# Kernel optimization log

Measured on AMD Instinct MI355X. Metric: run time of the kernel, lower is better.

## Reference

```python
import jax, jax.numpy as jnp
import numpy as np

D_MODEL = 1024
DFF = 4096
SPARSITY = 0.5
EPS = 1e-6


def layer_norm(x, gamma, beta):
    mu = jnp.mean(x, axis=-1, keepdims=True)
    var = jnp.mean(jnp.square(x - mu), axis=-1, keepdims=True)
    return (x - mu) * jax.lax.rsqrt(var + EPS) * gamma + beta


def setup_inputs() -> dict:
    key = jax.random.key(0)
    ks = jax.random.split(key, 8)
    B, S, d, f = 4, 2048, D_MODEL, DFF
    s = 1.0 / np.sqrt(d)
    return {
        "x": jax.random.normal(ks[0], (B, S, d), dtype=jnp.float32),
        "Wq": jax.random.normal(ks[1], (d, d), dtype=jnp.float32) * s,
        "bq": jnp.zeros((d,), jnp.float32),
        "Wk": jax.random.normal(ks[2], (d, d), dtype=jnp.float32) * s,
        "bk": jnp.zeros((d,), jnp.float32),
        "Wv": jax.random.normal(ks[3], (d, d), dtype=jnp.float32) * s,
        "bv": jnp.zeros((d,), jnp.float32),
        "W1": jax.random.normal(ks[4], (d, f), dtype=jnp.float32) * s,
        "b1": jnp.zeros((f,), jnp.float32),
        "W2": jax.random.normal(ks[5], (f, d), dtype=jnp.float32) * (1.0 / np.sqrt(f)),
        "b2": jnp.zeros((d,), jnp.float32),
        "gamma1": jnp.ones((d,), jnp.float32),
        "beta1": jnp.zeros((d,), jnp.float32),
        "gamma2": jnp.ones((d,), jnp.float32),
        "beta2": jnp.zeros((d,), jnp.float32),
    }


def reference(x, Wq, bq, Wk, bk, Wv, bv, W1, b1, W2, b2, gamma1, beta1, gamma2, beta2):
    B, S, d = x.shape
    q = x @ Wq + bq
    k = x @ Wk + bk
    v = x @ Wv + bv
    # scores: [B, S, S], scaled by sqrt(d_model)
    scores = jnp.einsum("bqd,bkd->bqk", q, k) / jnp.sqrt(jnp.float32(d))
    # top-k sparsification: keep scores >= row-wise k-th largest, else 0
    topk = int(SPARSITY * S)
    top_vals = jax.lax.top_k(scores, topk)[0]  # sorted descending
    threshold = top_vals[..., -1:]
    sparse_scores = jnp.where(scores >= threshold, scores, jnp.zeros_like(scores))
    attn = jax.nn.softmax(sparse_scores, axis=-1)
    attn_out = jnp.einsum("bqk,bkd->bqd", attn, v)
    out1 = layer_norm(x + attn_out, gamma1, beta1)
    ffn = jax.nn.relu(out1 @ W1 + b1) @ W2 + b2
    return layer_norm(out1 + ffn, gamma2, beta2)
```

## Files before the change

kernel.cpp:

```cpp
#include <hip/hip_runtime.h>
#include <cstdint>

typedef unsigned short u16;
typedef __attribute__((ext_vector_type(8))) short s16x8;
typedef __attribute__((ext_vector_type(4))) unsigned short u16x4;
typedef __attribute__((ext_vector_type(4))) float f32x4;

__device__ __forceinline__ u16 f2bf(float f) {
  union { float f; uint32_t u; } c; c.f = f;
  uint32_t r = c.u + 0x7FFFu + ((c.u >> 16) & 1u);
  return (u16)(r >> 16);
}
__device__ __forceinline__ float bf2f(u16 b) {
  union { uint32_t u; float f; } c; c.u = ((uint32_t)b) << 16;
  return c.f;
}
__device__ __forceinline__ float wave_sum_f(float v) {
#pragma unroll
  for (int o = 32; o > 0; o >>= 1) v += __shfl_xor(v, o);
  return v;
}
__device__ __forceinline__ float wave_max_f(float v) {
#pragma unroll
  for (int o = 32; o > 0; o >>= 1) v = fmaxf(v, __shfl_xor(v, o));
  return v;
}
__device__ __forceinline__ void gload16(const u16* g, u16* l) {
  __builtin_amdgcn_global_load_lds(
      (const __attribute__((address_space(1))) unsigned int*)g,
      (__attribute__((address_space(3))) unsigned int*)l,
      16, 0, 0);
}

__global__ __launch_bounds__(256)
void cast_f32_bf16(const float* __restrict__ in, u16* __restrict__ out) {
  long i = ((long)blockIdx.x * 256 + threadIdx.x) * 4;
  f32x4 v = *(const f32x4*)(in + i);
  u16x4 o;
#pragma unroll
  for (int j = 0; j < 4; ++j) o[j] = f2bf(v[j]);
  *(u16x4*)(out + i) = o;
}

__global__ __launch_bounds__(256)
void concat3(const float* __restrict__ a, const float* __restrict__ b,
             const float* __restrict__ c, float* __restrict__ o) {
  int i = blockIdx.x * 256 + threadIdx.x;
  o[i] = i < 1024 ? a[i] : (i < 2048 ? b[i - 1024] : c[i - 2048]);
}

__global__ __launch_bounds__(256)
void transpose_cast_f32_bf16(const float* __restrict__ in, u16* __restrict__ out,
                             int R, int C) {
  __shared__ float tile[32][33];
  int r0 = blockIdx.y * 32, c0 = blockIdx.x * 32;
  int tid = threadIdx.x;
  int tr = tid >> 3, tc4 = (tid & 7) * 4;
  f32x4 v = *(const f32x4*)(in + (long)(r0 + tr) * C + c0 + tc4);
#pragma unroll
  for (int j = 0; j < 4; ++j) tile[tr][tc4 + j] = v[j];
  __syncthreads();
  u16x4 o;
#pragma unroll
  for (int j = 0; j < 4; ++j) o[j] = f2bf(tile[tc4 + j][tr]);
  *(u16x4*)(out + (long)(c0 + tr) * R + r0 + tc4) = o;
}

__global__ __launch_bounds__(256)
void transpose_bf16(const u16* __restrict__ in, u16* __restrict__ out,
                    int R, int C, int in_rs, long in_batch, long out_batch) {
  __shared__ u16 tile[32][36];
  const long zin = (long)blockIdx.z * in_batch;
  const long zout = (long)blockIdx.z * out_batch;
  int r0 = blockIdx.y * 32, c0 = blockIdx.x * 32;
  int tid = threadIdx.x;
  int tr = tid >> 3, tc4 = (tid & 7) * 4;
  u16x4 v = *(const u16x4*)(in + zin + (long)(r0 + tr) * in_rs + c0 + tc4);
#pragma unroll
  for (int j = 0; j < 4; ++j) tile[tr][tc4 + j] = v[j];
  __syncthreads();
  u16x4 o;
#pragma unroll
  for (int j = 0; j < 4; ++j) o[j] = tile[tc4 + j][tr];
  *(u16x4*)(out + zout + (long)(c0 + tr) * R + r0 + tc4) = o;
}

#define TBM 256
#define TBK 64

enum { EPI_BF16_BIAS = 0, EPI_BF16_SCALE = 1, EPI_F32 = 2,
       EPI_RELU_BF16_BIAS = 3, EPI_F32_BIAS_RESID = 4 };

#define QUAD(MFA)                                                             \
  _Pragma("unroll")                                                           \
  for (int mf = (MFA); mf < (MFA) + 2; ++mf)                                  \
    _Pragma("unroll")                                                         \
    for (int nf = 0; nf < 4; ++nf) {                                          \
      acc[mf][nf] = __builtin_amdgcn_mfma_f32_16x16x32_bf16(                  \
          af[mf][0], bfr[nf][0], acc[mf][nf], 0, 0, 0);                       \
      acc[mf][nf] = __builtin_amdgcn_mfma_f32_16x16x32_bf16(                  \
          af[mf][1], bfr[nf][1], acc[mf][nf], 0, 0, 0);                       \
    }

template <int BN_, int EPI>
__global__ __launch_bounds__(512, 2)
void gemm2p(const u16* __restrict__ A, const u16* __restrict__ Bt,
            const float* __restrict__ bias, const float* __restrict__ resid,
            void* __restrict__ Cout, int M, int N, int K, int lda, int ldb,
            int tx, int ty, long long batchA, long long batchB, long long batchC,
            float scale) {
  constexpr int MF = (BN_ == 256) ? 8 : 4;
  constexpr int NBI = BN_ / 128;
  __shared__ u16 As[2][TBM * TBK];
  __shared__ u16 Bs[2][BN_ * TBK];

  const int nwg = gridDim.x;
  const int orig = blockIdx.x;
  const int q = nwg >> 3, r = nwg & 7;
  const int xcd = orig & 7, idx = orig >> 3;
  const int wg = (xcd < r ? xcd * (q + 1) : r * (q + 1) + (xcd - r) * q) + idx;
  const int bx = wg % tx;
  const int tmp = wg / tx;
  const int by = tmp % ty;
  const int b  = tmp / ty;

  const u16* Ab = A + (long)b * batchA;
  const u16* Bb = Bt + (long)b * batchB;
  const int row0 = by * TBM;
  const int col0 = bx * BN_;
  const int tid = threadIdx.x;
  const int lane = tid & 63, wid = tid >> 6;
  const int wm = (BN_ == 256) ? (wid >> 2) : (wid >> 1);
  const int wn = (BN_ == 256) ? (wid & 3) : (wid & 1);
  const int rowW = (BN_ == 256) ? wm * 128 : wm * 64;
  const int l15 = lane & 15, g = lane >> 4;

  const int sr = lane >> 3;
  const int sc = ((lane & 7) ^ sr) * 8;
  const int wrow = wid * 8 + sr;

  const int c0 = ((0 + g) ^ (l15 & 7)) * 8;
  const int c1 = ((4 + g) ^ (l15 & 7)) * 8;

  auto stageA = [&](int h, int kt, int bf_) {
#pragma unroll
    for (int j = 0; j < 2; ++j)
      gload16(Ab + (size_t)(row0 + h * 128 + j * 64 + wrow) * lda + kt * TBK + sc,
              &As[bf_][(h * 128 + j * 64 + wid * 8) * TBK]);
  };
  auto stageB = [&](int h, int kt, int bf_) {
#pragma unroll
    for (int j = 0; j < NBI; ++j)
      gload16(Bb + (size_t)(col0 + h * (BN_ / 2) + j * 64 + wrow) * ldb + kt * TBK + sc,
              &Bs[bf_][(h * (BN_ / 2) + j * 64 + wid * 8) * TBK]);
  };

  s16x8 af[MF][2];
  s16x8 bfr[4][2];
  f32x4 acc[MF][4] = {};
  const int nt = K / TBK;

  stageA(0, 0, 0); stageA(1, 0, 0);
  stageB(0, 0, 0); stageB(1, 0, 0);
  if (nt > 1) {
    stageA(0, 1, 1); stageA(1, 1, 1);
    stageB(0, 1, 1); stageB(1, 1, 1);
    if constexpr (BN_ == 256) asm volatile("s_waitcnt vmcnt(8)" ::: "memory");
    else                      asm volatile("s_waitcnt vmcnt(6)" ::: "memory");
  } else {
    asm volatile("s_waitcnt vmcnt(0)" ::: "memory");
  }
  __builtin_amdgcn_s_barrier();

  for (int t = 0; t < nt; ++t) {
    const int cur = t & 1;
    const u16* Asc = &As[cur][0];
    const u16* Bsc = &Bs[cur][0];

#pragma unroll
    for (int nf = 0; nf < 4; ++nf) {
      const int rb = (wn * 64 + nf * 16 + l15) * TBK;
      bfr[nf][0] = *(const s16x8*)(Bsc + rb + c0);
      bfr[nf][1] = *(const s16x8*)(Bsc + rb + c1);
    }
#pragma unroll
    for (int mf = 0; mf < MF; ++mf) {
      const int rb = (rowW + mf * 16 + l15) * TBK;
      af[mf][0] = *(const s16x8*)(Asc + rb + c0);
      af[mf][1] = *(const s16x8*)(Asc + rb + c1);
    }
    asm volatile("s_waitcnt lgkmcnt(0)" ::: "memory");
    __builtin_amdgcn_sched_barrier(0);
    __builtin_amdgcn_s_barrier();

    if (t + 2 < nt) { stageB(0, t + 2, cur); stageB(1, t + 2, cur); }
    __builtin_amdgcn_s_setprio(1);
    QUAD(0)
    if constexpr (MF == 8) { QUAD(2) }
    __builtin_amdgcn_s_setprio(0);
    if (t + 2 < nt) { stageA(0, t + 2, cur); stageA(1, t + 2, cur); }
    __builtin_amdgcn_s_setprio(1);
    if constexpr (MF == 8) { QUAD(4) QUAD(6) }
    else                   { QUAD(2) }
    __builtin_amdgcn_s_setprio(0);

    if (t + 1 < nt) {
      if (t + 2 < nt) {
        if constexpr (BN_ == 256) asm volatile("s_waitcnt vmcnt(8)" ::: "memory");
        else                      asm volatile("s_waitcnt vmcnt(6)" ::: "memory");
      } else {
        asm volatile("s_waitcnt vmcnt(0)" ::: "memory");
      }
      __builtin_amdgcn_s_barrier();
    }
  }

  const long cb = (long)b * batchC;
#pragma unroll
  for (int mf = 0; mf < MF; ++mf) {
    const int rbase = row0 + rowW + mf * 16 + g * 4;
#pragma unroll
    for (int nf = 0; nf < 4; ++nf) {
      const int col = col0 + wn * 64 + nf * 16 + l15;
#pragma unroll
      for (int rr = 0; rr < 4; ++rr) {
        const long cidx = cb + (long)(rbase + rr) * N + col;
        float v = acc[mf][nf][rr];
        if (EPI == EPI_BF16_BIAS) {
          ((u16*)Cout)[cidx] = f2bf(v + bias[col]);
        } else if (EPI == EPI_BF16_SCALE) {
          ((u16*)Cout)[cidx] = f2bf(v * scale);
        } else if (EPI == EPI_F32) {
          ((float*)Cout)[cidx] = v;
        } else if (EPI == EPI_RELU_BF16_BIAS) {
          ((u16*)Cout)[cidx] = f2bf(fmaxf(v + bias[col], 0.0f));
        } else {
          ((float*)Cout)[cidx] = v + bias[col] + resid[cidx];
        }
      }
    }
  }
}

__global__ __launch_bounds__(256)
void topk_softmax(const u16* __restrict__ scores, u16* __restrict__ P, int topk) {
  const int lane = threadIdx.x & 63, wid = threadIdx.x >> 6;
  const long row = (long)blockIdx.x * 4 + wid;
  const long rowoff = row * 2048;

  float v[32]; uint32_t kv[32];
  const uint32_t* src = (const uint32_t*)(scores + rowoff);
#pragma unroll
  for (int j = 0; j < 16; ++j) {
    uint32_t w = src[j * 64 + lane];
    v[2 * j]     = bf2f((u16)(w & 0xFFFFu));
    v[2 * j + 1] = bf2f((u16)(w >> 16));
  }
#pragma unroll
  for (int j = 0; j < 32; ++j) {
    union { float f; uint32_t u; } c; c.f = v[j];
    kv[j] = (c.u & 0x80000000u) ? ~c.u : (c.u | 0x80000000u);
  }
  float m = v[0];
#pragma unroll
  for (int j = 1; j < 32; ++j) m = fmaxf(m, v[j]);
  m = wave_max_f(m);

  uint32_t cur = 0;
  for (int bit = 31; bit >= 0; --bit) {
    const uint32_t cand = cur | (1u << bit);
    int c = 0;
#pragma unroll
    for (int j = 0; j < 32; ++j)
      c += (int)__popcll(__ballot(kv[j] >= cand));
    if (c >= topk) cur = cand;
  }

  const float mm = fmaxf(m, 0.0f);
  float p[32], s = 0.0f;
#pragma unroll
  for (int j = 0; j < 32; ++j) {
    float val = (kv[j] >= cur) ? v[j] : 0.0f;
    p[j] = __expf(val - mm);
    s += p[j];
  }
  s = wave_sum_f(s);
  const float inv = 1.0f / s;
  uint32_t* dst = (uint32_t*)(P + rowoff);
#pragma unroll
  for (int j = 0; j < 16; ++j) {
    uint32_t w = (uint32_t)f2bf(p[2 * j] * inv) |
                 ((uint32_t)f2bf(p[2 * j + 1] * inv) << 16);
    dst[j * 64 + lane] = w;
  }
}

__global__ __launch_bounds__(256)
void add_ln(const float* __restrict__ a, const float* __restrict__ r,
            const float* __restrict__ gamma, const float* __restrict__ beta,
            float* __restrict__ outf, u16* __restrict__ outb) {
  const long off = (long)blockIdx.x * 1024;
  const int tid = threadIdx.x, lane = tid & 63, wid = tid >> 6;
  __shared__ float sred[4];
  float x[4];
#pragma unroll
  for (int j = 0; j < 4; ++j) {
    int col = j * 256 + tid;
    float t = a[off + col];
    if (r) t += r[off + col];
    x[j] = t;
  }
  float s = x[0] + x[1] + x[2] + x[3];
  s = wave_sum_f(s);
  if (lane == 0) sred[wid] = s;
  __syncthreads();
  float mu = (sred[0] + sred[1] + sred[2] + sred[3]) * (1.0f / 1024.0f);
  __syncthreads();
  float qv = 0.0f;
#pragma unroll
  for (int j = 0; j < 4; ++j) { float d = x[j] - mu; qv += d * d; }
  qv = wave_sum_f(qv);
  if (lane == 0) sred[wid] = qv;
  __syncthreads();
  float var = (sred[0] + sred[1] + sred[2] + sred[3]) * (1.0f / 1024.0f);
  float inv = rsqrtf(var + 1e-6f);
#pragma unroll
  for (int j = 0; j < 4; ++j) {
    int col = j * 256 + tid;
    float o = (x[j] - mu) * inv * gamma[col] + beta[col];
    if (outf) outf[off + col] = o;
    if (outb) outb[off + col] = f2bf(o);
  }
}

extern "C" void kernel_launch(void* const* d_in, const int* in_sizes, int n_in,
                              void* d_out, int out_size, void* d_ws, size_t ws_size,
                              hipStream_t stream) {
  const float* x   = (const float*)d_in[0];
  const float* Wq  = (const float*)d_in[1];
  const float* bq  = (const float*)d_in[2];
  const float* Wk  = (const float*)d_in[3];
  const float* bk  = (const float*)d_in[4];
  const float* Wv  = (const float*)d_in[5];
  const float* bv  = (const float*)d_in[6];
  const float* W1  = (const float*)d_in[7];
  const float* b1  = (const float*)d_in[8];
  const float* W2  = (const float*)d_in[9];
  const float* b2  = (const float*)d_in[10];
  const float* g1  = (const float*)d_in[11];
  const float* be1 = (const float*)d_in[12];
  const float* g2  = (const float*)d_in[13];
  const float* be2 = (const float*)d_in[14];

  const int Bz = 4, S = 2048, Dm = 1024, Ff = 4096;
  const int M = Bz * S;
  const int N3 = 3 * Dm;

  char* ws = (char*)d_ws;
  const size_t MBy = 1024u * 1024u;
  u16*  wqkvT  = (u16*)(ws + 0 * MBy);
  u16*  w1T    = (u16*)(ws + 6 * MBy);
  u16*  w2T    = (u16*)(ws + 14 * MBy);
  u16*  xbf    = (u16*)(ws + 23 * MBy);
  u16*  qkv    = (u16*)(ws + 39 * MBy);
  u16*  vT     = (u16*)(ws + 87 * MBy);
  float* bqkv  = (float*)(ws + 103 * MBy);
  u16*  scores = (u16*)(ws + 103 * MBy);
  u16*  P      = (u16*)(ws + 167 * MBy);
  float* attn  = (float*)(ws + 103 * MBy);
  float* out1  = (float*)(ws + 135 * MBy);
  u16*  out1b  = (u16*)(ws + 23 * MBy);
  u16*  hbf    = (u16*)(ws + 39 * MBy);
  float* y     = (float*)(ws + 167 * MBy);

  dim3 blk(256);
  dim3 blk8(512);

  cast_f32_bf16<<<dim3((unsigned)((long)M * Dm / 1024)), blk, 0, stream>>>(x, xbf);
  transpose_cast_f32_bf16<<<dim3(Dm / 32, Dm / 32), blk, 0, stream>>>(Wq, wqkvT, Dm, Dm);
  transpose_cast_f32_bf16<<<dim3(Dm / 32, Dm / 32), blk, 0, stream>>>(Wk, wqkvT + 1024 * 1024, Dm, Dm);
  transpose_cast_f32_bf16<<<dim3(Dm / 32, Dm / 32), blk, 0, stream>>>(Wv, wqkvT + 2048 * 1024, Dm, Dm);
  transpose_cast_f32_bf16<<<dim3(Ff / 32, Dm / 32), blk, 0, stream>>>(W1, w1T, Dm, Ff);
  transpose_cast_f32_bf16<<<dim3(Dm / 32, Ff / 32), blk, 0, stream>>>(W2, w2T, Ff, Dm);
  concat3<<<dim3(12), blk, 0, stream>>>(bq, bk, bv, bqkv);

  gemm2p<128, EPI_BF16_BIAS><<<dim3(24 * 32), blk8, 0, stream>>>(
      xbf, wqkvT, bqkv, nullptr, qkv, M, N3, Dm, Dm, Dm, 24, 32, 0, 0, 0, 1.0f);

  transpose_bf16<<<dim3(Dm / 32, S / 32, Bz), blk, 0, stream>>>(
      qkv + 2048, vT, S, Dm, N3, (long)S * N3, (long)Dm * S);

  gemm2p<256, EPI_BF16_SCALE><<<dim3(8 * 8 * Bz), blk8, 0, stream>>>(
      qkv, qkv + 1024, nullptr, nullptr, scores, S, S, Dm, N3, N3, 8, 8,
      (long long)S * N3, (long long)S * N3, (long long)S * S, 0.03125f);

  topk_softmax<<<dim3(Bz * S / 4), blk, 0, stream>>>(scores, P, S / 2);

  gemm2p<128, EPI_F32><<<dim3(8 * 8 * Bz), blk8, 0, stream>>>(
      P, vT, nullptr, nullptr, attn, S, Dm, S, S, S, 8, 8,
      (long long)S * S, (long long)Dm * S, (long long)S * Dm, 1.0f);

  add_ln<<<dim3(M), blk, 0, stream>>>(x, attn, g1, be1, out1, out1b);

  gemm2p<256, EPI_RELU_BF16_BIAS><<<dim3(16 * 32), blk8, 0, stream>>>(
      out1b, w1T, b1, nullptr, hbf, M, Ff, Dm, Dm, Dm, 16, 32, 0, 0, 0, 1.0f);

  gemm2p<128, EPI_F32_BIAS_RESID><<<dim3(8 * 32), blk8, 0, stream>>>(
      hbf, w2T, b2, out1, y, M, Dm, Ff, Ff, Ff, 8, 32, 0, 0, 0, 1.0f);

  add_ln<<<dim3(M), blk, 0, stream>>>(y, nullptr, g2, be2, (float*)d_out, nullptr);
}
```

Before: 408.7 us.

## Shrink GEMM tiles to BK=32, BN=128 and raise occupancy to 4 blocks

Replaces the templated GEMM (BN 128/256, BK 64) with a single 256x128 tile and K-step 32, with a new LDS swizzle and one MFMA per fragment per step. Shared memory per block drops, so launch bounds are raised to 4 blocks per CU for more latency hiding. The scores and FFN1 GEMMs now launch twice as many blocks. This trades lower per-block reuse and more barriers per K element for higher occupancy and a fuller grid.

```diff
diff --git a/kernel.cpp b/kernel.cpp
--- a/kernel.cpp
+++ b/kernel.cpp
@@ -86,33 +86,29 @@
 }
 
 #define TBM 256
-#define TBK 64
+#define TBN 128
+#define TBK 32
 
 enum { EPI_BF16_BIAS = 0, EPI_BF16_SCALE = 1, EPI_F32 = 2,
        EPI_RELU_BF16_BIAS = 3, EPI_F32_BIAS_RESID = 4 };
 
-#define QUAD(MFA)                                                             \
+#define QUAD2(MFA)                                                            \
   _Pragma("unroll")                                                           \
   for (int mf = (MFA); mf < (MFA) + 2; ++mf)                                  \
     _Pragma("unroll")                                                         \
-    for (int nf = 0; nf < 4; ++nf) {                                          \
+    for (int nf = 0; nf < 4; ++nf)                                            \
       acc[mf][nf] = __builtin_amdgcn_mfma_f32_16x16x32_bf16(                  \
-          af[mf][0], bfr[nf][0], acc[mf][nf], 0, 0, 0);                       \
-      acc[mf][nf] = __builtin_amdgcn_mfma_f32_16x16x32_bf16(                  \
-          af[mf][1], bfr[nf][1], acc[mf][nf], 0, 0, 0);                       \
-    }
-
-template <int BN_, int EPI>
-__global__ __launch_bounds__(512, 2)
+          af[mf], bfr[nf], acc[mf][nf], 0, 0, 0);
+
+template <int EPI>
+__global__ __launch_bounds__(512, 4)
 void gemm2p(const u16* __restrict__ A, const u16* __restrict__ Bt,
             const float* __restrict__ bias, const float* __restrict__ resid,
             void* __restrict__ Cout, int M, int N, int K, int lda, int ldb,
             int tx, int ty, long long batchA, long long batchB, long long batchC,
             float scale) {
-  constexpr int MF = (BN_ == 256) ? 8 : 4;
-  constexpr int NBI = BN_ / 128;
   __shared__ u16 As[2][TBM * TBK];
-  __shared__ u16 Bs[2][BN_ * TBK];
+  __shared__ u16 Bs[2][TBN * TBK];
 
   const int nwg = gridDim.x;
   const int orig = blockIdx.x;
@@ -127,46 +123,39 @@
   const u16* Ab = A + (long)b * batchA;
   const u16* Bb = Bt + (long)b * batchB;
   const int row0 = by * TBM;
-  const int col0 = bx * BN_;
+  const int col0 = bx * TBN;
   const int tid = threadIdx.x;
   const int lane = tid & 63, wid = tid >> 6;
-  const int wm = (BN_ == 256) ? (wid >> 2) : (wid >> 1);
-  const int wn = (BN_ == 256) ? (wid & 3) : (wid & 1);
-  const int rowW = (BN_ == 256) ? wm * 128 : wm * 64;
+  const int wm = wid >> 1, wn = wid & 1;
+  const int rowW = wm * 64;
   const int l15 = lane & 15, g = lane >> 4;
 
-  const int sr = lane >> 3;
-  const int sc = ((lane & 7) ^ sr) * 8;
-  const int wrow = wid * 8 + sr;
-
-  const int c0 = ((0 + g) ^ (l15 & 7)) * 8;
-  const int c1 = ((4 + g) ^ (l15 & 7)) * 8;
-
-  auto stageA = [&](int h, int kt, int bf_) {
+  const int sr = lane >> 2;
+  const int sc = ((lane & 3) ^ ((lane >> 3) & 3)) * 8;
+  const int wrow = wid * 16 + sr;
+
+  const int coff = (g ^ ((l15 >> 1) & 3)) * 8;
+
+  auto stageA = [&](int kt, int bf_) {
 #pragma unroll
     for (int j = 0; j < 2; ++j)
-      gload16(Ab + (size_t)(row0 + h * 128 + j * 64 + wrow) * lda + kt * TBK + sc,
-              &As[bf_][(h * 128 + j * 64 + wid * 8) * TBK]);
+      gload16(Ab + (size_t)(row0 + j * 128 + wrow) * lda + kt * TBK + sc,
+              &As[bf_][(j * 128 + wid * 16) * TBK]);
   };
-  auto stageB = [&](int h, int kt, int bf_) {
-#pragma unroll
-    for (int j = 0; j < NBI; ++j)
-      gload16(Bb + (size_t)(col0 + h * (BN_ / 2) + j * 64 + wrow) * ldb + kt * TBK + sc,
-              &Bs[bf_][(h * (BN_ / 2) + j * 64 + wid * 8) * TBK]);
+  auto stageB = [&](int kt, int bf_) {
+    gload16(Bb + (size_t)(col0 + wrow) * ldb + kt * TBK + sc,
+            &Bs[bf_][(wid * 16) * TBK]);
   };
 
-  s16x8 af[MF][2];
-  s16x8 bfr[4][2];
-  f32x4 acc[MF][4] = {};
+  s16x8 af[4];
+  s16x8 bfr[4];
+  f32x4 acc[4][4] = {};
   const int nt = K / TBK;
 
-  stageA(0, 0, 0); stageA(1, 0, 0);
-  stageB(0, 0, 0); stageB(1, 0, 0);
+  stageA(0, 0); stageB(0, 0);
   if (nt > 1) {
-    stageA(0, 1, 1); stageA(1, 1, 1);
-    stageB(0, 1, 1); stageB(1, 1, 1);
-    if constexpr (BN_ == 256) asm volatile("s_waitcnt vmcnt(8)" ::: "memory");
-    else                      asm volatile("s_waitcnt vmcnt(6)" ::: "memory");
+    stageA(1, 1); stageB(1, 1);
+    asm volatile("s_waitcnt vmcnt(3)" ::: "memory");
   } else {
     asm volatile("s_waitcnt vmcnt(0)" ::: "memory");
   }
@@ -178,46 +167,34 @@
     const u16* Bsc = &Bs[cur][0];
 
 #pragma unroll
-    for (int nf = 0; nf < 4; ++nf) {
-      const int rb = (wn * 64 + nf * 16 + l15) * TBK;
-      bfr[nf][0] = *(const s16x8*)(Bsc + rb + c0);
-      bfr[nf][1] = *(const s16x8*)(Bsc + rb + c1);
-    }
-#pragma unroll
-    for (int mf = 0; mf < MF; ++mf) {
-      const int rb = (rowW + mf * 16 + l15) * TBK;
-      af[mf][0] = *(const s16x8*)(Asc + rb + c0);
-      af[mf][1] = *(const s16x8*)(Asc + rb + c1);
-    }
+    for (int nf = 0; nf < 4; ++nf)
+      bfr[nf] = *(const s16x8*)(Bsc + (wn * 64 + nf * 16 + l15) * TBK + coff);
+#pragma unroll
+    for (int mf = 0; mf < 4; ++mf)
+      af[mf] = *(const s16x8*)(Asc + (rowW + mf * 16 + l15) * TBK + coff);
     asm volatile("s_waitcnt lgkmcnt(0)" ::: "memory");
     __builtin_amdgcn_sched_barrier(0);
     __builtin_amdgcn_s_barrier();
 
-    if (t + 2 < nt) { stageB(0, t + 2, cur); stageB(1, t + 2, cur); }
+    if (t + 2 < nt) stageB(t + 2, cur);
     __builtin_amdgcn_s_setprio(1);
-    QUAD(0)
-    if constexpr (MF == 8) { QUAD(2) }
+    QUAD2(0)
     __builtin_amdgcn_s_setprio(0);
-    if (t + 2 < nt) { stageA(0, t + 2, cur); stageA(1, t + 2, cur); }
+    if (t + 2 < nt) stageA(t + 2, cur);
     __builtin_amdgcn_s_setprio(1);
-    if constexpr (MF == 8) { QUAD(4) QUAD(6) }
-    else                   { QUAD(2) }
+    QUAD2(2)
     __builtin_amdgcn_s_setprio(0);
 
     if (t + 1 < nt) {
-      if (t + 2 < nt) {
-        if constexpr (BN_ == 256) asm volatile("s_waitcnt vmcnt(8)" ::: "memory");
-        else                      asm volatile("s_waitcnt vmcnt(6)" ::: "memory");
-      } else {
-        asm volatile("s_waitcnt vmcnt(0)" ::: "memory");
-      }
+      if (t + 2 < nt) asm volatile("s_waitcnt vmcnt(3)" ::: "memory");
+      else            asm volatile("s_waitcnt vmcnt(0)" ::: "memory");
       __builtin_amdgcn_s_barrier();
     }
   }
 
   const long cb = (long)b * batchC;
 #pragma unroll
-  for (int mf = 0; mf < MF; ++mf) {
+  for (int mf = 0; mf < 4; ++mf) {
     const int rbase = row0 + rowW + mf * 16 + g * 4;
 #pragma unroll
     for (int nf = 0; nf < 4; ++nf) {
@@ -384,28 +361,28 @@
   transpose_cast_f32_bf16<<<dim3(Dm / 32, Ff / 32), blk, 0, stream>>>(W2, w2T, Ff, Dm);
   concat3<<<dim3(12), blk, 0, stream>>>(bq, bk, bv, bqkv);
 
-  gemm2p<128, EPI_BF16_BIAS><<<dim3(24 * 32), blk8, 0, stream>>>(
+  gemm2p<EPI_BF16_BIAS><<<dim3(24 * 32), blk8, 0, stream>>>(
       xbf, wqkvT, bqkv, nullptr, qkv, M, N3, Dm, Dm, Dm, 24, 32, 0, 0, 0, 1.0f);
 
   transpose_bf16<<<dim3(Dm / 32, S / 32, Bz), blk, 0, stream>>>(
       qkv + 2048, vT, S, Dm, N3, (long)S * N3, (long)Dm * S);
 
-  gemm2p<256, EPI_BF16_SCALE><<<dim3(8 * 8 * Bz), blk8, 0, stream>>>(
-      qkv, qkv + 1024, nullptr, nullptr, scores, S, S, Dm, N3, N3, 8, 8,
+  gemm2p<EPI_BF16_SCALE><<<dim3(16 * 8 * Bz), blk8, 0, stream>>>(
+      qkv, qkv + 1024, nullptr, nullptr, scores, S, S, Dm, N3, N3, 16, 8,
       (long long)S * N3, (long long)S * N3, (long long)S * S, 0.03125f);
 
   topk_softmax<<<dim3(Bz * S / 4), blk, 0, stream>>>(scores, P, S / 2);
 
-  gemm2p<128, EPI_F32><<<dim3(8 * 8 * Bz), blk8, 0, stream>>>(
+  gemm2p<EPI_F32><<<dim3(8 * 8 * Bz), blk8, 0, stream>>>(
       P, vT, nullptr, nullptr, attn, S, Dm, S, S, S, 8, 8,
       (long long)S * S, (long long)Dm * S, (long long)S * Dm, 1.0f);
 
   add_ln<<<dim3(M), blk, 0, stream>>>(x, attn, g1, be1, out1, out1b);
 
-  gemm2p<256, EPI_RELU_BF16_BIAS><<<dim3(16 * 32), blk8, 0, stream>>>(
-      out1b, w1T, b1, nullptr, hbf, M, Ff, Dm, Dm, Dm, 16, 32, 0, 0, 0, 1.0f);
-
-  gemm2p<128, EPI_F32_BIAS_RESID><<<dim3(8 * 32), blk8, 0, stream>>>(
+  gemm2p<EPI_RELU_BF16_BIAS><<<dim3(32 * 32), blk8, 0, stream>>>(
+      out1b, w1T, b1, nullptr, hbf, M, Ff, Dm, Dm, Dm, 32, 32, 0, 0, 0, 1.0f);
+
+  gemm2p<EPI_F32_BIAS_RESID><<<dim3(8 * 32), blk8, 0, stream>>>(
       hbf, w2T, b2, out1, y, M, Dm, Ff, Ff, Ff, 8, 32, 0, 0, 0, 1.0f);
 
   add_ln<<<dim3(M), blk, 0, stream>>>(y, nullptr, g2, be2, (float*)d_out, nullptr);
```

Measured after the change: 442.6 us. 1.08x slower.
